# Kernel tuning notes

Hardware: AMD Instinct MI355X
Metric: run time of the kernel (lower is better)

The kernel has to match this reference:

```python
import jax, jax.numpy as jnp
import numpy as np

N = 50000   # nodes
E = 600000  # edges / hyperedge incidences
D = 128     # node_in_dim
H = 128     # hidden_dim
TAU = 0.5
ALPHA = 0.5
LAM = 0.5

_PARAM_SHAPES = [('Wq0', (1, H)), ('bq0', (H,)), ('W0', (D, H)), ('b0', (H,)),
                 ('Whq0', (1, H)), ('bhq0', (H,)), ('Wh0', (D, H)), ('bh0', (H,)),
                 ('Wf0', (H, H)), ('bf0', (H,)), ('Wfh0', (H, H)), ('bfh0', (H,)),
                 ('aq0', (H,)), ('a0', (H,)), ('ahq0', (H,)), ('ah0', (H,)),
                 ('aq_', (H,)), ('a_', (H,)), ('ahq_', (H,)), ('ah_', (H,)),
                 ('Wlq', (1, H)), ('blq', (H,)), ('Wlf', (D, H)), ('blf', (H,)),
                 ('Wm1', (H, H)), ('bm1', (H,)), ('Wm2', (H, H)), ('bm2', (H,))]


def setup_inputs() -> dict:
    key = jax.random.key(0)
    ks = jax.random.split(key, 8 + len(_PARAM_SHAPES))
    inp = {}
    inp['feats'] = jax.random.normal(ks[0], (N, D), dtype=jnp.float32)
    inp['edge_index'] = jax.random.randint(ks[1], (2, E), 0, N).astype(jnp.int32)
    inp['edge_index_aug'] = jax.random.randint(ks[2], (2, E), 0, N).astype(jnp.int32)
    inp['pos'] = jax.random.randint(ks[3], (100,), 1, N).astype(jnp.int32)
    inp['q'] = 0
    for i, (nm, sh) in enumerate(_PARAM_SHAPES):
        inp[nm] = jax.random.normal(ks[4 + i], sh, dtype=jnp.float32) * 0.05
    return inp


def _forward(feats, Wq0, bq0, W0, b0, Whq0, bhq0, Wh0, bh0, Wf0, bf0, Wfh0, bfh0,
             aq0, a0, ahq0, ah0, aq_, a_, ahq_, ah_, Wlq, blq, Wlf, blf,
             Wm1, bm1, Wm2, bm2, edge_index, edge_index_aug, q, pos):
    # ---- GCNConv (PyG default: add self-loops + symmetric normalization) ----
    sl = jnp.arange(N, dtype=edge_index.dtype)
    src = jnp.concatenate([edge_index[0], sl])
    dst = jnp.concatenate([edge_index[1], sl])
    deg = jax.ops.segment_sum(jnp.ones(src.shape[0], jnp.float32), dst, num_segments=N)
    dinv = jax.lax.rsqrt(deg)  # deg >= 1 thanks to self-loops
    enorm = dinv[src] * dinv[dst]

    def gcn(x, W, b):
        xw = x @ W
        return jax.ops.segment_sum(xw[src] * enorm[:, None], dst, num_segments=N) + b

    # ---- HypergraphConv (PyG, no attention): X' = D^-1 H B^-1 H^T X W ----
    node = edge_index_aug[0]
    he = edge_index_aug[1]
    Be = jax.ops.segment_sum(jnp.ones((E,), jnp.float32), he, num_segments=N)
    Dn = jax.ops.segment_sum(jnp.ones((E,), jnp.float32), node, num_segments=N)
    Binv = jnp.where(Be > 0, 1.0 / Be, 0.0)
    Dninv = jnp.where(Dn > 0, 1.0 / Dn, 0.0)

    def hg(x, W, b):
        xw = x @ W
        me = jax.ops.segment_sum(xw[node], he, num_segments=N) * Binv[:, None]
        return jax.ops.segment_sum(me[he], node, num_segments=N) * Dninv[:, None] + b

    # ---- attention-weighted fusion of two views (softmax over 2 logits) ----
    def fuse(a, b, wa, wb):
        att = jax.nn.softmax(jnp.stack([a @ wa, b @ wb], axis=1), axis=1)  # [N,2]
        return att[:, 0:1] * a + att[:, 1:2] * b

    querys = jnp.zeros((N, 1), jnp.float32).at[q].set(1.0)
    hq = jax.nn.relu(gcn(querys, Wq0, bq0))
    h = jax.nn.relu(gcn(feats, W0, b0))
    hf = fuse(hq, h, aq0, a0)
    h_augq = jax.nn.relu(hg(querys, Whq0, bhq0))
    h_aug = jax.nn.relu(hg(feats, Wh0, bh0))
    h_augf = fuse(h_augq, h_aug, ahq0, ah0)
    querys2 = querys @ Wlq + blq
    feats2 = feats @ Wlf + blf
    hf_ = fuse(querys2, feats2, aq_, a_)
    hf = jax.nn.relu(hf + gcn(hf_, Wf0, bf0))
    hfh_ = fuse(querys2, feats2, ahq_, ah_)
    h_augf = jax.nn.relu(h_augf + hg(hfh_, Wfh0, bfh0))

    def mlp(x):
        return jax.nn.relu(x @ Wm1 + bm1) @ Wm2 + bm2

    z = mlp(hf)
    z_aug = mlp(h_augf)

    # ---- Contra loss ----
    def expcos(v, M):
        num = M @ v
        den = jnp.maximum(jnp.linalg.norm(M, axis=1) * jnp.linalg.norm(v), 1e-8)
        return jnp.exp(num / den / TAU)

    sim1 = expcos(z[q], z)
    sim_aug1 = expcos(z_aug[q], z_aug)
    sim2 = expcos(z[q], z_aug)
    sim_aug2 = expcos(z_aug[q], z)
    mask = jnp.zeros((N,), bool).at[pos].set(True).at[q].set(False)
    nmask = jnp.sum(mask).astype(jnp.float32)

    def nlm(s):  # mean over positives of -log(s_i / sum(s))
        r = jnp.log(jnp.sum(s)) - jnp.log(s)
        return jnp.sum(jnp.where(mask, r, 0.0)) / nmask

    loss_intra = 0.5 * (nlm(sim1) + nlm(sim_aug1))
    loss_inter = 0.5 * (nlm(sim2) + nlm(sim_aug2))
    z_unsup = jnp.log(jnp.sum(sim2)) - jnp.log(sim2[q])
    z_aug_unsup = jnp.log(jnp.sum(sim_aug2)) - jnp.log(sim_aug2[q])
    loss_unsup = 0.5 * z_unsup + 0.5 * z_aug_unsup
    return loss_intra + ALPHA * loss_inter + LAM * loss_unsup


def reference(feats, Wq0, bq0, W0, b0, Whq0, bhq0, Wh0, bh0, Wf0, bf0, Wfh0, bfh0,
              aq0, a0, ahq0, ah0, aq_, a_, ahq_, ah_, Wlq, blq, Wlf, blf,
              Wm1, bm1, Wm2, bm2, edge_index, edge_index_aug, q, pos):
    return _forward(feats, Wq0, bq0, W0, b0, Whq0, bhq0, Wh0, bh0, Wf0, bf0, Wfh0, bfh0,
                    aq0, a0, ahq0, ah0, aq_, a_, ahq_, ah_, Wlq, blq, Wlf, blf,
                    Wm1, bm1, Wm2, bm2, edge_index, edge_index_aug, q, pos)
```

## Files before the change

kernel.cpp:

```cpp
#include <hip/hip_runtime.h>

#define NN 50000
#define EE 600000
#define HH 128
#define TAU_INV 2.0f
#define PSZ 6250
#define CAP 48

typedef __attribute__((ext_vector_type(8))) short short8;
typedef __attribute__((ext_vector_type(4))) float f32x4;
typedef __attribute__((ext_vector_type(2))) float floatx2;

__device__ __forceinline__ float wsum64(float v) {
#pragma unroll
  for (int m = 32; m >= 1; m >>= 1) v += __shfl_xor(v, m, 64);
  return v;
}
__device__ __forceinline__ unsigned short f2bf(float f) {
  unsigned u = __builtin_bit_cast(unsigned, f);
  u = u + 0x7FFFu + ((u >> 16) & 1u);
  return (unsigned short)(u >> 16);
}
__device__ __forceinline__ float bf2f(unsigned short h) {
  unsigned u = ((unsigned)h) << 16;
  return __builtin_bit_cast(float, u);
}
__device__ __forceinline__ unsigned char fp8_enc1(float v) {
  int p = __builtin_amdgcn_cvt_pk_fp8_f32(v, v, 0, false);
  return (unsigned char)(p & 0xFF);
}
__device__ __forceinline__ void fp8x8_dec(uint2 v, float* f) {
  floatx2 a = __builtin_amdgcn_cvt_pk_f32_fp8(v.x, false);
  floatx2 b = __builtin_amdgcn_cvt_pk_f32_fp8(v.x, true);
  floatx2 c = __builtin_amdgcn_cvt_pk_f32_fp8(v.y, false);
  floatx2 d = __builtin_amdgcn_cvt_pk_f32_fp8(v.y, true);
  f[0] = a.x; f[1] = a.y; f[2] = b.x; f[3] = b.y;
  f[4] = c.x; f[5] = c.y; f[6] = d.x; f[7] = d.y;
}
__device__ __forceinline__ uint2 fp8x8_enc(const float* f) {
  int w0 = __builtin_amdgcn_cvt_pk_fp8_f32(f[0], f[1], 0, false);
  w0 = __builtin_amdgcn_cvt_pk_fp8_f32(f[2], f[3], w0, true);
  int w1 = __builtin_amdgcn_cvt_pk_fp8_f32(f[4], f[5], 0, false);
  w1 = __builtin_amdgcn_cvt_pk_fp8_f32(f[6], f[7], w1, true);
  return make_uint2((unsigned)w0, (unsigned)w1);
}

__global__ void fill_k(const int* __restrict__ ei, const int* __restrict__ ea,
                       const int* __restrict__ qp, int* __restrict__ cursor,
                       unsigned short* __restrict__ slotsA, unsigned short* __restrict__ slotsB,
                       unsigned short* __restrict__ slotsC, float* __restrict__ cntq) {
  const int p = blockIdx.x & 7;
  const int lo = p * PSZ, hi = lo + PSZ;
  const int q = *qp;
  const int stride = (gridDim.x >> 3) * 256;
  for (int e = (blockIdx.x >> 3) * 256 + threadIdx.x; e < EE; e += stride) {
    int dst = __builtin_nontemporal_load(ei + EE + e);
    int node = __builtin_nontemporal_load(ea + e);
    int he = __builtin_nontemporal_load(ea + EE + e);
    if (dst >= lo && dst < hi) {
      int src = __builtin_nontemporal_load(ei + e);
      int idx = atomicAdd(&cursor[dst], 1);
      if (idx < CAP) slotsA[dst * CAP + idx] = (unsigned short)src;
    }
    if (he >= lo && he < hi) {
      int idx = atomicAdd(&cursor[NN + he], 1);
      if (idx < CAP) slotsB[he * CAP + idx] = (unsigned short)node;
      if (node == q) atomicAdd(&cntq[he], 1.0f);
    }
    if (node >= lo && node < hi) {
      int idx = atomicAdd(&cursor[2 * NN + node], 1);
      if (idx < CAP) slotsC[node * CAP + idx] = (unsigned short)he;
    }
  }
}

__global__ void derive_k(const int* __restrict__ cursor, float* __restrict__ dinv,
                         float* __restrict__ Binv, float* __restrict__ Dninv,
                         const int* __restrict__ pos, const int* __restrict__ qp,
                         int* __restrict__ maskI) {
  int i = blockIdx.x * 256 + threadIdx.x;
  if (i < NN) {
    dinv[i] = rsqrtf((float)(cursor[i] + 1));
    int b = cursor[NN + i];
    Binv[i] = (b > 0) ? 1.0f / (float)b : 0.0f;
    int d = cursor[2 * NN + i];
    Dninv[i] = (d > 0) ? 1.0f / (float)d : 0.0f;
  }
  if (blockIdx.x == 0) {
    int t = threadIdx.x;
    if (t < 100) maskI[pos[t]] = 1;
    __syncthreads();
    if (t == 0) maskI[*qp] = 0;
  }
}

__global__ void shq_k(const int* __restrict__ ei, const int* __restrict__ ea,
                      const int* __restrict__ qp, const float* __restrict__ dinv,
                      const float* __restrict__ Binv, const float* __restrict__ cntq,
                      float* __restrict__ s_hq, float* __restrict__ s_hgq) {
  int e = blockIdx.x * 256 + threadIdx.x;
  if (e >= EE) return;
  int q = *qp;
  int src = __builtin_nontemporal_load(ei + e);
  if (src == q) {
    int dst = __builtin_nontemporal_load(ei + EE + e);
    atomicAdd(&s_hq[dst], dinv[q] * dinv[dst]);
  }
  int he = __builtin_nontemporal_load(ea + EE + e);
  float cq = cntq[he];
  if (cq != 0.0f) {
    int node = __builtin_nontemporal_load(ea + e);
    atomicAdd(&s_hgq[node], Binv[he] * cq);
  }
  if (e == 0) atomicAdd(&s_hq[q], dinv[q] * dinv[q]);
}

__global__ void pack_k(const float* __restrict__ W0, const float* __restrict__ Wh0,
                       const float* __restrict__ Wlf, const float* __restrict__ Wf0,
                       const float* __restrict__ Wfh0, const float* __restrict__ Wm1,
                       const float* __restrict__ Wm2, unsigned short* __restrict__ out) {
  int tid = blockIdx.x * 256 + threadIdx.x;
  if (tid >= 7 * 2048) return;
  int mat = tid >> 11, r = tid & 2047;
  int s = r >> 9, c = (r >> 6) & 7, lane = r & 63;
  const float* W = (mat == 0) ? W0 : (mat == 1) ? Wh0 : (mat == 2) ? Wlf
                 : (mat == 3) ? Wf0 : (mat == 4) ? Wfh0 : (mat == 5) ? Wm1 : Wm2;
  int k0 = 32 * s + (lane >> 4) * 8;
  int n = 16 * c + (lane & 15);
  unsigned short* o = out + (size_t)tid * 8;
#pragma unroll
  for (int j = 0; j < 8; ++j) o[j] = f2bf(W[(k0 + j) * 128 + n]);
}

#define LDSW 136

template <bool BIAS, bool RELU, int OM>
__device__ __forceinline__ void gemm_core(const unsigned short* As, const short8* Wp,
                                          const float* bias, void* outv, int r0, int nrows,
                                          int tid) {
  const int wave = tid >> 6, lane = tid & 63;
  const int quad = lane >> 4, l15 = lane & 15;
  const int rw = r0 + wave * 16;
  f32x4 acc[8];
#pragma unroll
  for (int c = 0; c < 8; ++c) acc[c] = (f32x4){0.f, 0.f, 0.f, 0.f};
#pragma unroll
  for (int s = 0; s < 4; ++s) {
    short8 a = *(const short8*)&As[(wave * 16 + l15) * LDSW + s * 32 + quad * 8];
#pragma unroll
    for (int c = 0; c < 8; ++c) {
      short8 b = Wp[(s * 8 + c) * 64 + lane];
      acc[c] = __builtin_amdgcn_mfma_f32_16x16x32_bf16(a, b, acc[c], 0, 0, 0);
    }
  }
#pragma unroll
  for (int c = 0; c < 8; ++c) {
    int col = c * 16 + l15;
    float bv = BIAS ? bias[col] : 0.f;
#pragma unroll
    for (int r = 0; r < 4; ++r) {
      int grow = rw + quad * 4 + r;
      if (grow < nrows) {
        float v = acc[c][r] + bv;
        if (RELU) v = fmaxf(v, 0.f);
        if (OM == 2)
          ((unsigned char*)outv)[(size_t)grow * 256 + col] = fp8_enc1(v);
        else if (OM == 1)
          ((unsigned short*)outv)[(size_t)grow * 128 + col] = f2bf(v);
        else
          ((float*)outv)[(size_t)grow * 128 + col] = v;
      }
    }
  }
}

__device__ __forceinline__ void stage_bf16(const unsigned short* A, unsigned short* As,
                                           int r0, int nrows, int tid) {
#pragma unroll
  for (int t = 0; t < 4; ++t) {
    int v = t * 256 + tid;
    int row = v >> 4, cc = v & 15;
    int gr = r0 + row;
    uint4 val = make_uint4(0, 0, 0, 0);
    if (gr < nrows) val = ((const uint4*)A)[(size_t)gr * 16 + cc];
    *(uint4*)&As[row * LDSW + cc * 8] = val;
  }
}

template <bool BIAS, bool RELU, int OM>
__global__ __launch_bounds__(256) void gemm2_mfma(const unsigned short* __restrict__ A0,
                                                  const unsigned short* __restrict__ A1,
                                                  const short8* __restrict__ Wp0,
                                                  const short8* __restrict__ Wp1,
                                                  const float* __restrict__ b0,
                                                  const float* __restrict__ b1,
                                                  void* __restrict__ o0, void* __restrict__ o1,
                                                  int nrows, int nblk) {
  __shared__ unsigned short As[64 * LDSW];
  int b = blockIdx.x;
  const unsigned short* A = A0;
  const short8* Wp = Wp0;
  const float* bias = b0;
  void* o = o0;
  if (b >= nblk) {
    b -= nblk; A = A1; Wp = Wp1; bias = b1; o = o1;
  }
  const int r0 = b * 64;
  stage_bf16(A, As, r0, nrows, threadIdx.x);
  __syncthreads();
  gemm_core<BIAS, RELU, OM>(As, Wp, bias, o, r0, nrows, threadIdx.x);
}

__global__ __launch_bounds__(256) void gemm3_mfma(const float* __restrict__ A,
                                                  const short8* __restrict__ Wp,
                                                  const float* __restrict__ bias2,
                                                  unsigned char* __restrict__ p1,
                                                  unsigned char* __restrict__ p2,
                                                  unsigned short* __restrict__ out2,
                                                  int nrows) {
  __shared__ unsigned short As[64 * LDSW];
  const int tid = threadIdx.x;
  const int r0 = blockIdx.x * 64;
#pragma unroll
  for (int t = 0; t < 8; ++t) {
    int v = t * 256 + tid;
    int row = v >> 5, c4 = v & 31;
    int gr = r0 + row;
    float4 val = make_float4(0.f, 0.f, 0.f, 0.f);
    if (gr < nrows) val = ((const float4*)A)[(size_t)gr * 32 + c4];
    ushort4 o;
    o.x = f2bf(val.x); o.y = f2bf(val.y); o.z = f2bf(val.z); o.w = f2bf(val.w);
    *(ushort4*)&As[row * LDSW + c4 * 4] = o;
  }
  __syncthreads();
  const int wave = tid >> 6, lane = tid & 63;
  const int quad = lane >> 4, l15 = lane & 15;
  const int rw = r0 + wave * 16;
  f32x4 acc[3][8];
#pragma unroll
  for (int m = 0; m < 3; ++m)
#pragma unroll
    for (int c = 0; c < 8; ++c) acc[m][c] = (f32x4){0.f, 0.f, 0.f, 0.f};
#pragma unroll
  for (int s = 0; s < 4; ++s) {
    short8 a = *(const short8*)&As[(wave * 16 + l15) * LDSW + s * 32 + quad * 8];
#pragma unroll
    for (int m = 0; m < 3; ++m)
#pragma unroll
      for (int c = 0; c < 8; ++c) {
        short8 b = Wp[(size_t)m * 2048 + (s * 8 + c) * 64 + lane];
        acc[m][c] = __builtin_amdgcn_mfma_f32_16x16x32_bf16(a, b, acc[m][c], 0, 0, 0);
      }
  }
#pragma unroll
  for (int c = 0; c < 8; ++c) {
    int col = c * 16 + l15;
    float bv = bias2[col];
#pragma unroll
    for (int r = 0; r < 4; ++r) {
      int grow = rw + quad * 4 + r;
      if (grow < nrows) {
        p1[(size_t)grow * 256 + col] = fp8_enc1(acc[0][c][r]);
        p2[(size_t)grow * 256 + col] = fp8_enc1(acc[1][c][r]);
        out2[(size_t)grow * 128 + col] = f2bf(acc[2][c][r] + bv);
      }
    }
  }
}

template <int MODE, bool OUTFP8>
__device__ __forceinline__ void gpair_body(const uint2* __restrict__ xp,
                                           unsigned short* __restrict__ y1,
                                           unsigned short* __restrict__ y2,
                                           uint2* __restrict__ yp,
                                           const int* __restrict__ cnt,
                                           const unsigned short* __restrict__ slots,
                                           const float* __restrict__ wv, int blk) {
  int node = blk * 8 + (threadIdx.x >> 5);
  if (node >= NN) return;
  int l = threadIdx.x & 31;
  int st = node * CAP;
  int n = min(cnt[node], CAP);
  float acc[8];
#pragma unroll
  for (int i = 0; i < 8; ++i) acc[i] = 0.f;
  int p = 0;
  for (; p + 4 <= n; p += 4) {
    ushort4 s4 = *(const ushort4*)&slots[st + p];
    uint2 v0 = xp[(size_t)s4.x * 32 + l];
    uint2 v1 = xp[(size_t)s4.y * 32 + l];
    uint2 v2 = xp[(size_t)s4.z * 32 + l];
    uint2 v3 = xp[(size_t)s4.w * 32 + l];
    float f[8];
    if (MODE == 0) {
      float w0 = wv[s4.x], w1 = wv[s4.y], w2 = wv[s4.z], w3 = wv[s4.w];
      fp8x8_dec(v0, f);
#pragma unroll
      for (int i = 0; i < 8; ++i) acc[i] = fmaf(w0, f[i], acc[i]);
      fp8x8_dec(v1, f);
#pragma unroll
      for (int i = 0; i < 8; ++i) acc[i] = fmaf(w1, f[i], acc[i]);
      fp8x8_dec(v2, f);
#pragma unroll
      for (int i = 0; i < 8; ++i) acc[i] = fmaf(w2, f[i], acc[i]);
      fp8x8_dec(v3, f);
#pragma unroll
      for (int i = 0; i < 8; ++i) acc[i] = fmaf(w3, f[i], acc[i]);
    } else {
      fp8x8_dec(v0, f);
#pragma unroll
      for (int i = 0; i < 8; ++i) acc[i] += f[i];
      fp8x8_dec(v1, f);
#pragma unroll
      for (int i = 0; i < 8; ++i) acc[i] += f[i];
      fp8x8_dec(v2, f);
#pragma unroll
      for (int i = 0; i < 8; ++i) acc[i] += f[i];
      fp8x8_dec(v3, f);
#pragma unroll
      for (int i = 0; i < 8; ++i) acc[i] += f[i];
    }
  }
  for (; p < n; ++p) {
    int s = slots[st + p];
    uint2 v = xp[(size_t)s * 32 + l];
    float f[8];
    fp8x8_dec(v, f);
    if (MODE == 0) {
      float w = wv[s];
#pragma unroll
      for (int i = 0; i < 8; ++i) acc[i] = fmaf(w, f[i], acc[i]);
    } else {
#pragma unroll
      for (int i = 0; i < 8; ++i) acc[i] += f[i];
    }
  }
  float sc = wv[node];
  if (MODE == 0) {
    uint2 v = xp[(size_t)node * 32 + l];
    float f[8];
    fp8x8_dec(v, f);
#pragma unroll
    for (int i = 0; i < 8; ++i) acc[i] = sc * fmaf(sc, f[i], acc[i]);
  } else {
#pragma unroll
    for (int i = 0; i < 8; ++i) acc[i] *= sc;
  }
  if (OUTFP8) {
    yp[(size_t)node * 32 + l] = fp8x8_enc(acc);
  } else {
    unsigned short* y = (l < 16) ? y1 : y2;
    int cg = l & 15;
    uint4 o;
    o.x = ((unsigned)f2bf(acc[1]) << 16) | f2bf(acc[0]);
    o.y = ((unsigned)f2bf(acc[3]) << 16) | f2bf(acc[2]);
    o.z = ((unsigned)f2bf(acc[5]) << 16) | f2bf(acc[4]);
    o.w = ((unsigned)f2bf(acc[7]) << 16) | f2bf(acc[6]);
    *(uint4*)&y[(size_t)node * 128 + cg * 8] = o;
  }
}

__global__ void dgather12_k(const uint2* __restrict__ xp1, unsigned short* __restrict__ y1a,
                            unsigned short* __restrict__ y1b, const uint2* __restrict__ xp2,
                            uint2* __restrict__ yp3, const int* __restrict__ cursor,
                            const unsigned short* __restrict__ slotsA,
                            const unsigned short* __restrict__ slotsB,
                            const float* __restrict__ dinv, const float* __restrict__ Binv,
                            int nblk) {
  int b = blockIdx.x;
  if (b < nblk)
    gpair_body<0, false>(xp1, y1a, y1b, nullptr, cursor, slotsA, dinv, b);
  else
    gpair_body<1, true>(xp2, nullptr, nullptr, yp3, cursor + NN, slotsB, Binv, b - nblk);
}

__global__ void dgather3_k(const uint2* __restrict__ xp, unsigned short* __restrict__ y1,
                           unsigned short* __restrict__ y2, const int* __restrict__ cursor,
                           const unsigned short* __restrict__ slotsC,
                           const float* __restrict__ wv) {
  gpair_body<1, false>(xp, y1, y2, nullptr, cursor + 2 * NN, slotsC, wv, blockIdx.x);
}

__device__ __forceinline__ void fuse_add_body(const unsigned short* __restrict__ g,
                                              const unsigned short* __restrict__ gr,
                                              const float* __restrict__ svec,
                                              const float* __restrict__ dscale,
                                              const float* __restrict__ Wq,
                                              const float* __restrict__ bq,
                                              const float* __restrict__ bm,
                                              const float* __restrict__ aq,
                                              const float* __restrict__ am,
                                              const float* __restrict__ bres,
                                              unsigned short* __restrict__ out, int blk) {
  int row = blk * 4 + (threadIdx.x >> 6);
  if (row >= NN) return;
  int lane = threadIdx.x & 63;
  int c0 = lane, c1 = lane + 64;
  float s = svec[row];
  if (dscale) s *= dscale[row];
  float hq0 = fmaxf(fmaf(s, Wq[c0], bq[c0]), 0.f);
  float hq1 = fmaxf(fmaf(s, Wq[c1], bq[c1]), 0.f);
  float h0 = fmaxf(bf2f(g[(size_t)row * 128 + c0]) + bm[c0], 0.f);
  float h1 = fmaxf(bf2f(g[(size_t)row * 128 + c1]) + bm[c1], 0.f);
  float dq = wsum64(hq0 * aq[c0] + hq1 * aq[c1]);
  float dm = wsum64(h0 * am[c0] + h1 * am[c1]);
  float mx = fmaxf(dq, dm);
  float e0 = expf(dq - mx), e1 = expf(dm - mx);
  float w0 = e0 / (e0 + e1), w1 = 1.f - w0;
  float r0 = fmaxf(w0 * hq0 + w1 * h0 + bf2f(gr[(size_t)row * 128 + c0]) + bres[c0], 0.f);
  float r1 = fmaxf(w0 * hq1 + w1 * h1 + bf2f(gr[(size_t)row * 128 + c1]) + bres[c1], 0.f);
  out[(size_t)row * 128 + c0] = f2bf(r0);
  out[(size_t)row * 128 + c1] = f2bf(r1);
}

__global__ void fuse_add2_k(const unsigned short* gA, const unsigned short* grA,
                            const float* svA, const float* dsA, const float* WqA,
                            const float* bqA, const float* bmA, const float* aqA,
                            const float* amA, const float* brA, unsigned short* outA,
                            const unsigned short* gB, const unsigned short* grB,
                            const float* svB, const float* dsB, const float* WqB,
                            const float* bqB, const float* bmB, const float* aqB,
                            const float* amB, const float* brB, unsigned short* outB,
                            int nblk) {
  int b = blockIdx.x;
  if (b < nblk)
    fuse_add_body(gA, grA, svA, dsA, WqA, bqA, bmA, aqA, amA, brA, outA, b);
  else
    fuse_add_body(gB, grB, svB, dsB, WqB, bqB, bmB, aqB, amB, brB, outB, b - nblk);
}

__global__ void fuse2_k(const unsigned short* __restrict__ f2, const int* __restrict__ qp,
                        const float* __restrict__ Wlq, const float* __restrict__ blq,
                        const float* __restrict__ aq1, const float* __restrict__ a1,
                        const float* __restrict__ aq2, const float* __restrict__ a2,
                        unsigned short* __restrict__ out1, unsigned short* __restrict__ out2) {
  int row = blockIdx.x * 4 + (threadIdx.x >> 6);
  if (row >= NN) return;
  int lane = threadIdx.x & 63;
  int c0 = lane, c1 = lane + 64;
  int q = *qp;
  float q20 = blq[c0] + ((row == q) ? Wlq[c0] : 0.f);
  float q21 = blq[c1] + ((row == q) ? Wlq[c1] : 0.f);
  float f0 = bf2f(f2[(size_t)row * 128 + c0]);
  float f1 = bf2f(f2[(size_t)row * 128 + c1]);
  float dq1 = wsum64(q20 * aq1[c0] + q21 * aq1[c1]);
  float df1 = wsum64(f0 * a1[c0] + f1 * a1[c1]);
  float dq2 = wsum64(q20 * aq2[c0] + q21 * aq2[c1]);
  float df2 = wsum64(f0 * a2[c0] + f1 * a2[c1]);
  {
    float mx = fmaxf(dq1, df1);
    float e0 = expf(dq1 - mx), e1 = expf(df1 - mx);
    float w0 = e0 / (e0 + e1), w1 = 1.f - w0;
    out1[(size_t)row * 128 + c0] = f2bf(w0 * q20 + w1 * f0);
    out1[(size_t)row * 128 + c1] = f2bf(w0 * q21 + w1 * f1);
  }
  {
    float mx = fmaxf(dq2, df2);
    float e0 = expf(dq2 - mx), e1 = expf(df2 - mx);
    float w0 = e0 / (e0 + e1), w1 = 1.f - w0;
    out2[(size_t)row * 128 + c0] = f2bf(w0 * q20 + w1 * f0);
    out2[(size_t)row * 128 + c1] = f2bf(w0 * q21 + w1 * f1);
  }
}

__global__ void sim_k(const unsigned short* __restrict__ z,
                      const unsigned short* __restrict__ za, const int* __restrict__ qp,
                      float4* __restrict__ simbuf, float* __restrict__ scal_out) {
  int row = blockIdx.x * 4 + (threadIdx.x >> 6);
  if (row >= NN) return;
  int lane = threadIdx.x & 63;
  int c0 = lane, c1 = lane + 64;
  int q = *qp;
  float zi0 = bf2f(z[(size_t)row * 128 + c0]), zi1 = bf2f(z[(size_t)row * 128 + c1]);
  float zai0 = bf2f(za[(size_t)row * 128 + c0]), zai1 = bf2f(za[(size_t)row * 128 + c1]);
  float zq0 = bf2f(z[(size_t)q * 128 + c0]), zq1 = bf2f(z[(size_t)q * 128 + c1]);
  float zaq0 = bf2f(za[(size_t)q * 128 + c0]), zaq1 = bf2f(za[(size_t)q * 128 + c1]);
  float nzi = wsum64(zi0 * zi0 + zi1 * zi1);
  float nzai = wsum64(zai0 * zai0 + zai1 * zai1);
  float nzq = wsum64(zq0 * zq0 + zq1 * zq1);
  float nzaq = wsum64(zaq0 * zaq0 + zaq1 * zaq1);
  float d1 = wsum64(zi0 * zq0 + zi1 * zq1);
  float d2 = wsum64(zai0 * zaq0 + zai1 * zaq1);
  float d3 = wsum64(zai0 * zq0 + zai1 * zq1);
  float d4 = wsum64(zi0 * zaq0 + zi1 * zaq1);
  if (lane == 0) {
    float ni = sqrtf(nzi), nai = sqrtf(nzai);
    float nq = sqrtf(nzq), naq = sqrtf(nzaq);
    float c1_ = d1 / fmaxf(ni * nq, 1e-8f) * TAU_INV;
    float ca1 = d2 / fmaxf(nai * naq, 1e-8f) * TAU_INV;
    float c2_ = d3 / fmaxf(nai * nq, 1e-8f) * TAU_INV;
    float ca2 = d4 / fmaxf(ni * naq, 1e-8f) * TAU_INV;
    simbuf[row] = make_float4(c1_, ca1, c2_, ca2);
    if (row == q) {
      scal_out[9] = c2_;
      scal_out[10] = ca2;
    }
  }
}

__global__ __launch_bounds__(256) void reduce_sim_k(const float4* __restrict__ simbuf,
                                                    const int* __restrict__ maskI,
                                                    float* __restrict__ scal) {
  float acc[9];
#pragma unroll
  for (int i = 0; i < 9; ++i) acc[i] = 0.f;
  for (int row = blockIdx.x * 256 + threadIdx.x; row < NN; row += gridDim.x * 256) {
    float4 v = simbuf[row];
    acc[0] += expf(v.x);
    acc[1] += expf(v.y);
    acc[2] += expf(v.z);
    acc[3] += expf(v.w);
    if (maskI[row]) {
      acc[4] += v.x; acc[5] += v.y; acc[6] += v.z; acc[7] += v.w;
      acc[8] += 1.0f;
    }
  }
  __shared__ float s[9][4];
  int lane = threadIdx.x & 63, wv = threadIdx.x >> 6;
#pragma unroll
  for (int i = 0; i < 9; ++i) {
    float r = wsum64(acc[i]);
    if (lane == 0) s[i][wv] = r;
  }
  __syncthreads();
  if (threadIdx.x < 9) {
    float r = s[threadIdx.x][0] + s[threadIdx.x][1] + s[threadIdx.x][2] + s[threadIdx.x][3];
    atomicAdd(&scal[threadIdx.x], r);
  }
}

__global__ void final_k(const float* __restrict__ scal, float* __restrict__ out) {
  if (threadIdx.x != 0 || blockIdx.x != 0) return;
  float S1 = scal[0], Sa1 = scal[1], S2 = scal[2], Sa2 = scal[3];
  float L1 = scal[4], La1 = scal[5], L2 = scal[6], La2 = scal[7];
  float NM = scal[8], Q2 = scal[9], Qa2 = scal[10];
  float intra = 0.5f * ((logf(S1) - L1 / NM) + (logf(Sa1) - La1 / NM));
  float inter = 0.5f * ((logf(S2) - L2 / NM) + (logf(Sa2) - La2 / NM));
  float unsup = 0.5f * (logf(S2) - Q2) + 0.5f * (logf(Sa2) - Qa2);
  out[0] = intra + 0.5f * inter + 0.5f * unsup;
}

extern "C" void kernel_launch(void* const* d_in, const int* in_sizes, int n_in,
                              void* d_out, int out_size, void* d_ws, size_t ws_size,
                              hipStream_t stream) {
  const float* feats = (const float*)d_in[0];
  const int* ei = (const int*)d_in[1];
  const int* ea = (const int*)d_in[2];
  const int* pos = (const int*)d_in[3];
  const int* qp = (const int*)d_in[4];
  const float* Wq0 = (const float*)d_in[5];
  const float* bq0 = (const float*)d_in[6];
  const float* W0 = (const float*)d_in[7];
  const float* b0 = (const float*)d_in[8];
  const float* Whq0 = (const float*)d_in[9];
  const float* bhq0 = (const float*)d_in[10];
  const float* Wh0 = (const float*)d_in[11];
  const float* bh0 = (const float*)d_in[12];
  const float* Wf0 = (const float*)d_in[13];
  const float* bf0 = (const float*)d_in[14];
  const float* Wfh0 = (const float*)d_in[15];
  const float* bfh0 = (const float*)d_in[16];
  const float* aq0 = (const float*)d_in[17];
  const float* a0 = (const float*)d_in[18];
  const float* ahq0 = (const float*)d_in[19];
  const float* ah0 = (const float*)d_in[20];
  const float* aq_ = (const float*)d_in[21];
  const float* a_ = (const float*)d_in[22];
  const float* ahq_ = (const float*)d_in[23];
  const float* ah_ = (const float*)d_in[24];
  const float* Wlq = (const float*)d_in[25];
  const float* blq = (const float*)d_in[26];
  const float* Wlf = (const float*)d_in[27];
  const float* blf = (const float*)d_in[28];
  const float* Wm1 = (const float*)d_in[29];
  const float* bm1 = (const float*)d_in[30];
  const float* Wm2 = (const float*)d_in[31];
  const float* bm2 = (const float*)d_in[32];

  char* ws = (char*)d_ws;
  size_t off = 0;
  auto take = [&](size_t bytes) -> void* {
    void* p = ws + off;
    off = (off + bytes + 255) & ~(size_t)255;
    return p;
  };
  int* cursor3 = (int*)take(3 * NN * 4);
  int* maskI = (int*)take(NN * 4);
  float* s_hq = (float*)take(NN * 4);
  float* cntq = (float*)take(NN * 4);
  float* s_hgq = (float*)take(NN * 4);
  float* scal = (float*)take(64 * 4);
  size_t zero_end = off;
  unsigned short* slotsA = (unsigned short*)take((size_t)NN * CAP * 2);
  unsigned short* slotsB = (unsigned short*)take((size_t)NN * CAP * 2);
  unsigned short* slotsC = (unsigned short*)take((size_t)NN * CAP * 2);
  float* dinv = (float*)take(NN * 4);
  float* Binv = (float*)take(NN * 4);
  float* Dninv = (float*)take(NN * 4);
  float4* simbuf = (float4*)take((size_t)NN * 16);
  unsigned short* Wpack = (unsigned short*)take((size_t)7 * 16384 * 2);
  const size_t BFSZ = (size_t)NN * HH * 2;
  unsigned short* B0 = (unsigned short*)take(BFSZ);
  unsigned short* B1 = (unsigned short*)take(BFSZ);
  unsigned short* B2 = (unsigned short*)take(BFSZ);
  unsigned short* B3 = (unsigned short*)take(BFSZ);
  unsigned short* B4 = (unsigned short*)take(BFSZ);
  unsigned short* B5 = (unsigned short*)take(BFSZ);
  unsigned short* B6 = (unsigned short*)take(BFSZ);
  unsigned char* P1 = (unsigned char*)take((size_t)NN * 256);
  unsigned char* P2 = (unsigned char*)take((size_t)NN * 256);
  unsigned char* P3 = (unsigned char*)take((size_t)NN * 256);

  const int NB = (NN + 255) / 256;
  const int EB = (EE + 255) / 256;
  const int GMB = (NN + 63) / 64;
  const int GTB = (NN + 7) / 8;
  const int RB = (NN + 3) / 4;
  const short8* Wp = (const short8*)Wpack;

  hipMemsetAsync(d_ws, 0, zero_end, stream);
  fill_k<<<4096, 256, 0, stream>>>(ei, ea, qp, cursor3, slotsA, slotsB, slotsC, cntq);
  derive_k<<<NB, 256, 0, stream>>>(cursor3, dinv, Binv, Dninv, pos, qp, maskI);
  shq_k<<<EB, 256, 0, stream>>>(ei, ea, qp, dinv, Binv, cntq, s_hq, s_hgq);

  pack_k<<<(7 * 2048 + 255) / 256, 256, 0, stream>>>(W0, Wh0, Wlf, Wf0, Wfh0, Wm1, Wm2,
                                                     Wpack);
  gemm3_mfma<<<GMB, 256, 0, stream>>>(feats, Wp, blf, P1, P2, B6, NN);
  fuse2_k<<<RB, 256, 0, stream>>>(B6, qp, Wlq, blq, aq_, a_, ahq_, ah_, B3, B4);
  gemm2_mfma<false, false, 2><<<2 * GMB, 256, 0, stream>>>(
      B3, B4, Wp + (size_t)3 * 2048, Wp + (size_t)4 * 2048, nullptr, nullptr, P1 + 128,
      P2 + 128, NN, GMB);
  dgather12_k<<<2 * GTB, 256, 0, stream>>>((const uint2*)P1, B0, B1, (const uint2*)P2,
                                           (uint2*)P3, cursor3, slotsA, slotsB, dinv, Binv,
                                           GTB);
  dgather3_k<<<GTB, 256, 0, stream>>>((const uint2*)P3, B2, B5, cursor3, slotsC, Dninv);
  fuse_add2_k<<<2 * RB, 256, 0, stream>>>(
      B0, B1, s_hq, nullptr, Wq0, bq0, b0, aq0, a0, bf0, B3,
      B2, B5, s_hgq, Dninv, Whq0, bhq0, bh0, ahq0, ah0, bfh0, B4, RB);
  gemm2_mfma<true, true, 1><<<2 * GMB, 256, 0, stream>>>(
      B3, B4, Wp + (size_t)5 * 2048, Wp + (size_t)5 * 2048, bm1, bm1, B0, B1, NN, GMB);
  gemm2_mfma<true, false, 1><<<2 * GMB, 256, 0, stream>>>(
      B0, B1, Wp + (size_t)6 * 2048, Wp + (size_t)6 * 2048, bm2, bm2, B2, B5, NN, GMB);
  sim_k<<<RB, 256, 0, stream>>>(B2, B5, qp, simbuf, scal);
  reduce_sim_k<<<64, 256, 0, stream>>>(simbuf, maskI, scal);
  final_k<<<1, 64, 0, stream>>>(scal, (float*)d_out);
}
```

Measured before the change: 479.6 us.

## Merge independent GEMM and CSR fill, shq and fuse2 into shared launches

Independent stages are combined into single launches by splitting the grid. The feature GEMM (gemm3) runs alongside the edge slot fill, and the query-scatter kernel runs alongside the attention fuse2 kernel. This removes two launches and lets the compute-bound GEMM blocks overlap with the atomic-bound fill blocks. The GEMM's feature loads also become nontemporal. The fill kernel's stride is now fixed to FILLB, and the fused kernels carry a larger shared register and LDS footprint, which may lower occupancy for the lighter fill and shq blocks.

```diff
diff --git a/kernel.cpp b/kernel.cpp
--- a/kernel.cpp
+++ b/kernel.cpp
@@ -6,6 +6,7 @@
 #define TAU_INV 2.0f
 #define PSZ 6250
 #define CAP 48
+#define FILLB 4096
 
 typedef __attribute__((ext_vector_type(8))) short short8;
 typedef __attribute__((ext_vector_type(4))) float f32x4;
@@ -45,15 +46,20 @@
   return make_uint2((unsigned)w0, (unsigned)w1);
 }
 
-__global__ void fill_k(const int* __restrict__ ei, const int* __restrict__ ea,
-                       const int* __restrict__ qp, int* __restrict__ cursor,
-                       unsigned short* __restrict__ slotsA, unsigned short* __restrict__ slotsB,
-                       unsigned short* __restrict__ slotsC, float* __restrict__ cntq) {
-  const int p = blockIdx.x & 7;
+#define LDSW 136
+
+__device__ __forceinline__ void fill_body(const int* __restrict__ ei,
+                                          const int* __restrict__ ea,
+                                          const int* __restrict__ qp, int* __restrict__ cursor,
+                                          unsigned short* __restrict__ slotsA,
+                                          unsigned short* __restrict__ slotsB,
+                                          unsigned short* __restrict__ slotsC,
+                                          float* __restrict__ cntq, int bid) {
+  const int p = bid & 7;
   const int lo = p * PSZ, hi = lo + PSZ;
   const int q = *qp;
-  const int stride = (gridDim.x >> 3) * 256;
-  for (int e = (blockIdx.x >> 3) * 256 + threadIdx.x; e < EE; e += stride) {
+  const int stride = (FILLB >> 3) * 256;
+  for (int e = (bid >> 3) * 256 + threadIdx.x; e < EE; e += stride) {
     int dst = __builtin_nontemporal_load(ei + EE + e);
     int node = __builtin_nontemporal_load(ea + e);
     int he = __builtin_nontemporal_load(ea + EE + e);
@@ -72,6 +78,87 @@
       if (idx < CAP) slotsC[node * CAP + idx] = (unsigned short)he;
     }
   }
+}
+
+__device__ __forceinline__ void gemm3_body(const float* __restrict__ A,
+                                           const short8* __restrict__ Wp,
+                                           const float* __restrict__ bias2,
+                                           unsigned char* __restrict__ p1,
+                                           unsigned char* __restrict__ p2,
+                                           unsigned short* __restrict__ out2, int nrows,
+                                           int b) {
+  __shared__ unsigned short As[64 * LDSW];
+  const int tid = threadIdx.x;
+  const int r0 = b * 64;
+#pragma unroll
+  for (int t = 0; t < 8; ++t) {
+    int v = t * 256 + tid;
+    int row = v >> 5, c4 = v & 31;
+    int gr = r0 + row;
+    f32x4 val = (f32x4){0.f, 0.f, 0.f, 0.f};
+    if (gr < nrows) {
+      const f32x4* src = (const f32x4*)A + (size_t)gr * 32 + c4;
+      val = __builtin_nontemporal_load(src);
+    }
+    ushort4 o;
+    o.x = f2bf(val.x); o.y = f2bf(val.y); o.z = f2bf(val.z); o.w = f2bf(val.w);
+    *(ushort4*)&As[row * LDSW + c4 * 4] = o;
+  }
+  __syncthreads();
+  const int wave = tid >> 6, lane = tid & 63;
+  const int quad = lane >> 4, l15 = lane & 15;
+  const int rw = r0 + wave * 16;
+  f32x4 acc[3][8];
+#pragma unroll
+  for (int m = 0; m < 3; ++m)
+#pragma unroll
+    for (int c = 0; c < 8; ++c) acc[m][c] = (f32x4){0.f, 0.f, 0.f, 0.f};
+#pragma unroll
+  for (int s = 0; s < 4; ++s) {
+    short8 a = *(const short8*)&As[(wave * 16 + l15) * LDSW + s * 32 + quad * 8];
+#pragma unroll
+    for (int m = 0; m < 3; ++m)
+#pragma unroll
+      for (int c = 0; c < 8; ++c) {
+        short8 bb = Wp[(size_t)m * 2048 + (s * 8 + c) * 64 + lane];
+        acc[m][c] = __builtin_amdgcn_mfma_f32_16x16x32_bf16(a, bb, acc[m][c], 0, 0, 0);
+      }
+  }
+#pragma unroll
+  for (int c = 0; c < 8; ++c) {
+    int col = c * 16 + l15;
+    float bv = bias2[col];
+#pragma unroll
+    for (int r = 0; r < 4; ++r) {
+      int grow = rw + quad * 4 + r;
+      if (grow < nrows) {
+        p1[(size_t)grow * 256 + col] = fp8_enc1(acc[0][c][r]);
+        p2[(size_t)grow * 256 + col] = fp8_enc1(acc[1][c][r]);
+        out2[(size_t)grow * 128 + col] = f2bf(acc[2][c][r] + bv);
+      }
+    }
+  }
+}
+
+__global__ __launch_bounds__(256) void f1_k(const float* __restrict__ feats,
+                                            const short8* __restrict__ Wp,
+                                            const float* __restrict__ blf,
+                                            unsigned char* __restrict__ P1,
+                                            unsigned char* __restrict__ P2,
+                                            unsigned short* __restrict__ B6,
+                                            const int* __restrict__ ei,
+                                            const int* __restrict__ ea,
+                                            const int* __restrict__ qp,
+                                            int* __restrict__ cursor,
+                                            unsigned short* __restrict__ slotsA,
+                                            unsigned short* __restrict__ slotsB,
+                                            unsigned short* __restrict__ slotsC,
+                                            float* __restrict__ cntq, int gmb) {
+  int b = blockIdx.x;
+  if (b < gmb)
+    gemm3_body(feats, Wp, blf, P1, P2, B6, NN, b);
+  else
+    fill_body(ei, ea, qp, cursor, slotsA, slotsB, slotsC, cntq, b - gmb);
 }
 
 __global__ void derive_k(const int* __restrict__ cursor, float* __restrict__ dinv,
@@ -94,11 +181,14 @@
   }
 }
 
-__global__ void shq_k(const int* __restrict__ ei, const int* __restrict__ ea,
-                      const int* __restrict__ qp, const float* __restrict__ dinv,
-                      const float* __restrict__ Binv, const float* __restrict__ cntq,
-                      float* __restrict__ s_hq, float* __restrict__ s_hgq) {
-  int e = blockIdx.x * 256 + threadIdx.x;
+__device__ __forceinline__ void shq_body(const int* __restrict__ ei, const int* __restrict__ ea,
+                                         const int* __restrict__ qp,
+                                         const float* __restrict__ dinv,
+                                         const float* __restrict__ Binv,
+                                         const float* __restrict__ cntq,
+                                         float* __restrict__ s_hq, float* __restrict__ s_hgq,
+                                         int bid) {
+  int e = bid * 256 + threadIdx.x;
   if (e >= EE) return;
   int q = *qp;
   int src = __builtin_nontemporal_load(ei + e);
@@ -113,6 +203,69 @@
     atomicAdd(&s_hgq[node], Binv[he] * cq);
   }
   if (e == 0) atomicAdd(&s_hq[q], dinv[q] * dinv[q]);
+}
+
+__device__ __forceinline__ void fuse2_body(const unsigned short* __restrict__ f2,
+                                           const int* __restrict__ qp,
+                                           const float* __restrict__ Wlq,
+                                           const float* __restrict__ blq,
+                                           const float* __restrict__ aq1,
+                                           const float* __restrict__ a1,
+                                           const float* __restrict__ aq2,
+                                           const float* __restrict__ a2,
+                                           unsigned short* __restrict__ out1,
+                                           unsigned short* __restrict__ out2, int bid) {
+  int row = bid * 4 + (threadIdx.x >> 6);
+  if (row >= NN) return;
+  int lane = threadIdx.x & 63;
+  int c0 = lane, c1 = lane + 64;
+  int q = *qp;
+  float q20 = blq[c0] + ((row == q) ? Wlq[c0] : 0.f);
+  float q21 = blq[c1] + ((row == q) ? Wlq[c1] : 0.f);
+  float f0 = bf2f(f2[(size_t)row * 128 + c0]);
+  float f1 = bf2f(f2[(size_t)row * 128 + c1]);
+  float dq1 = wsum64(q20 * aq1[c0] + q21 * aq1[c1]);
+  float df1 = wsum64(f0 * a1[c0] + f1 * a1[c1]);
+  float dq2 = wsum64(q20 * aq2[c0] + q21 * aq2[c1]);
+  float df2 = wsum64(f0 * a2[c0] + f1 * a2[c1]);
+  {
+    float mx = fmaxf(dq1, df1);
+    float e0 = expf(dq1 - mx), e1 = expf(df1 - mx);
+    float w0 = e0 / (e0 + e1), w1 = 1.f - w0;
+    out1[(size_t)row * 128 + c0] = f2bf(w0 * q20 + w1 * f0);
+    out1[(size_t)row * 128 + c1] = f2bf(w0 * q21 + w1 * f1);
+  }
+  {
+    float mx = fmaxf(dq2, df2);
+    float e0 = expf(dq2 - mx), e1 = expf(df2 - mx);
+    float w0 = e0 / (e0 + e1), w1 = 1.f - w0;
+    out2[(size_t)row * 128 + c0] = f2bf(w0 * q20 + w1 * f0);
+    out2[(size_t)row * 128 + c1] = f2bf(w0 * q21 + w1 * f1);
+  }
+}
+
+__global__ __launch_bounds__(256) void f2_k(const int* __restrict__ ei,
+                                            const int* __restrict__ ea,
+                                            const int* __restrict__ qp,
+                                            const float* __restrict__ dinv,
+                                            const float* __restrict__ Binv,
+                                            const float* __restrict__ cntq,
+                                            float* __restrict__ s_hq,
+                                            float* __restrict__ s_hgq,
+                                            const unsigned short* __restrict__ B6,
+                                            const float* __restrict__ Wlq,
+                                            const float* __restrict__ blq,
+                                            const float* __restrict__ aq_,
+                                            const float* __restrict__ a_,
+                                            const float* __restrict__ ahq_,
+                                            const float* __restrict__ ah_,
+                                            unsigned short* __restrict__ B3,
+                                            unsigned short* __restrict__ B4, int eb) {
+  int b = blockIdx.x;
+  if (b < eb)
+    shq_body(ei, ea, qp, dinv, Binv, cntq, s_hq, s_hgq, b);
+  else
+    fuse2_body(B6, qp, Wlq, blq, aq_, a_, ahq_, ah_, B3, B4, b - eb);
 }
 
 __global__ void pack_k(const float* __restrict__ W0, const float* __restrict__ Wh0,
@@ -131,8 +284,6 @@
 #pragma unroll
   for (int j = 0; j < 8; ++j) o[j] = f2bf(W[(k0 + j) * 128 + n]);
 }
-
-#define LDSW 136
 
 template <bool BIAS, bool RELU, int OM>
 __device__ __forceinline__ void gemm_core(const unsigned short* As, const short8* Wp,
@@ -209,63 +360,6 @@
   stage_bf16(A, As, r0, nrows, threadIdx.x);
   __syncthreads();
   gemm_core<BIAS, RELU, OM>(As, Wp, bias, o, r0, nrows, threadIdx.x);
-}
-
-__global__ __launch_bounds__(256) void gemm3_mfma(const float* __restrict__ A,
-                                                  const short8* __restrict__ Wp,
-                                                  const float* __restrict__ bias2,
-                                                  unsigned char* __restrict__ p1,
-                                                  unsigned char* __restrict__ p2,
-                                                  unsigned short* __restrict__ out2,
-                                                  int nrows) {
-  __shared__ unsigned short As[64 * LDSW];
-  const int tid = threadIdx.x;
-  const int r0 = blockIdx.x * 64;
-#pragma unroll
-  for (int t = 0; t < 8; ++t) {
-    int v = t * 256 + tid;
-    int row = v >> 5, c4 = v & 31;
-    int gr = r0 + row;
-    float4 val = make_float4(0.f, 0.f, 0.f, 0.f);
-    if (gr < nrows) val = ((const float4*)A)[(size_t)gr * 32 + c4];
-    ushort4 o;
-    o.x = f2bf(val.x); o.y = f2bf(val.y); o.z = f2bf(val.z); o.w = f2bf(val.w);
-    *(ushort4*)&As[row * LDSW + c4 * 4] = o;
-  }
-  __syncthreads();
-  const int wave = tid >> 6, lane = tid & 63;
-  const int quad = lane >> 4, l15 = lane & 15;
-  const int rw = r0 + wave * 16;
-  f32x4 acc[3][8];
-#pragma unroll
-  for (int m = 0; m < 3; ++m)
-#pragma unroll
-    for (int c = 0; c < 8; ++c) acc[m][c] = (f32x4){0.f, 0.f, 0.f, 0.f};
-#pragma unroll
-  for (int s = 0; s < 4; ++s) {
-    short8 a = *(const short8*)&As[(wave * 16 + l15) * LDSW + s * 32 + quad * 8];
-#pragma unroll
-    for (int m = 0; m < 3; ++m)
-#pragma unroll
-      for (int c = 0; c < 8; ++c) {
-        short8 b = Wp[(size_t)m * 2048 + (s * 8 + c) * 64 + lane];
-        acc[m][c] = __builtin_amdgcn_mfma_f32_16x16x32_bf16(a, b, acc[m][c], 0, 0, 0);
-      }
-  }
-#pragma unroll
-  for (int c = 0; c < 8; ++c) {
-    int col = c * 16 + l15;
-    float bv = bias2[col];
-#pragma unroll
-    for (int r = 0; r < 4; ++r) {
-      int grow = rw + quad * 4 + r;
-      if (grow < nrows) {
-        p1[(size_t)grow * 256 + col] = fp8_enc1(acc[0][c][r]);
-        p2[(size_t)grow * 256 + col] = fp8_enc1(acc[1][c][r]);
-        out2[(size_t)grow * 128 + col] = f2bf(acc[2][c][r] + bv);
-      }
-    }
-  }
 }
 
 template <int MODE, bool OUTFP8>
@@ -427,40 +521,6 @@
     fuse_add_body(gA, grA, svA, dsA, WqA, bqA, bmA, aqA, amA, brA, outA, b);
   else
     fuse_add_body(gB, grB, svB, dsB, WqB, bqB, bmB, aqB, amB, brB, outB, b - nblk);
-}
-
-__global__ void fuse2_k(const unsigned short* __restrict__ f2, const int* __restrict__ qp,
-                        const float* __restrict__ Wlq, const float* __restrict__ blq,
-                        const float* __restrict__ aq1, const float* __restrict__ a1,
-                        const float* __restrict__ aq2, const float* __restrict__ a2,
-                        unsigned short* __restrict__ out1, unsigned short* __restrict__ out2) {
-  int row = blockIdx.x * 4 + (threadIdx.x >> 6);
-  if (row >= NN) return;
-  int lane = threadIdx.x & 63;
-  int c0 = lane, c1 = lane + 64;
-  int q = *qp;
-  float q20 = blq[c0] + ((row == q) ? Wlq[c0] : 0.f);
-  float q21 = blq[c1] + ((row == q) ? Wlq[c1] : 0.f);
-  float f0 = bf2f(f2[(size_t)row * 128 + c0]);
-  float f1 = bf2f(f2[(size_t)row * 128 + c1]);
-  float dq1 = wsum64(q20 * aq1[c0] + q21 * aq1[c1]);
-  float df1 = wsum64(f0 * a1[c0] + f1 * a1[c1]);
-  float dq2 = wsum64(q20 * aq2[c0] + q21 * aq2[c1]);
-  float df2 = wsum64(f0 * a2[c0] + f1 * a2[c1]);
-  {
-    float mx = fmaxf(dq1, df1);
-    float e0 = expf(dq1 - mx), e1 = expf(df1 - mx);
-    float w0 = e0 / (e0 + e1), w1 = 1.f - w0;
-    out1[(size_t)row * 128 + c0] = f2bf(w0 * q20 + w1 * f0);
-    out1[(size_t)row * 128 + c1] = f2bf(w0 * q21 + w1 * f1);
-  }
-  {
-    float mx = fmaxf(dq2, df2);
-    float e0 = expf(dq2 - mx), e1 = expf(df2 - mx);
-    float w0 = e0 / (e0 + e1), w1 = 1.f - w0;
-    out2[(size_t)row * 128 + c0] = f2bf(w0 * q20 + w1 * f0);
-    out2[(size_t)row * 128 + c1] = f2bf(w0 * q21 + w1 * f1);
-  }
 }
 
 __global__ void sim_k(const unsigned short* __restrict__ z,
@@ -619,14 +679,13 @@
   const short8* Wp = (const short8*)Wpack;
 
   hipMemsetAsync(d_ws, 0, zero_end, stream);
-  fill_k<<<4096, 256, 0, stream>>>(ei, ea, qp, cursor3, slotsA, slotsB, slotsC, cntq);
-  derive_k<<<NB, 256, 0, stream>>>(cursor3, dinv, Binv, Dninv, pos, qp, maskI);
-  shq_k<<<EB, 256, 0, stream>>>(ei, ea, qp, dinv, Binv, cntq, s_hq, s_hgq);
-
   pack_k<<<(7 * 2048 + 255) / 256, 256, 0, stream>>>(W0, Wh0, Wlf, Wf0, Wfh0, Wm1, Wm2,
                                                      Wpack);
-  gemm3_mfma<<<GMB, 256, 0, stream>>>(feats, Wp, blf, P1, P2, B6, NN);
-  fuse2_k<<<RB, 256, 0, stream>>>(B6, qp, Wlq, blq, aq_, a_, ahq_, ah_, B3, B4);
+  f1_k<<<GMB + FILLB, 256, 0, stream>>>(feats, Wp, blf, P1, P2, B6, ei, ea, qp, cursor3,
+                                        slotsA, slotsB, slotsC, cntq, GMB);
+  derive_k<<<NB, 256, 0, stream>>>(cursor3, dinv, Binv, Dninv, pos, qp, maskI);
+  f2_k<<<EB + RB, 256, 0, stream>>>(ei, ea, qp, dinv, Binv, cntq, s_hq, s_hgq, B6, Wlq,
+                                    blq, aq_, a_, ahq_, ah_, B3, B4, EB);
   gemm2_mfma<false, false, 2><<<2 * GMB, 256, 0, stream>>>(
       B3, B4, Wp + (size_t)3 * 2048, Wp + (size_t)4 * 2048, nullptr, nullptr, P1 + 128,
       P2 + 128, NN, GMB);
```

Result: slower. 540.6 us (+12.7%).
